# Kernel optimization log

Hardware: AMD Instinct MI355X
Metric: run time of the kernel (lower is better)

Reference implementation:

```python
import jax, jax.numpy as jnp
import numpy as np

TAU_PLUS = 0.02
TAU_MINUS = 0.02
TAU_X = 0.101
A_TRIPLET = 0.0065
HOMEOSTATIC_RATE = 0.1
DT = 0.001
SPIKE_P = 0.05  # spike probability used to binarize inputs


def setup_inputs() -> dict:
    key = jax.random.key(0)
    k1, k2, k3 = jax.random.split(key, 3)
    B, P, Q, T = 16, 2048, 2048, 256
    pre_spikes = (jax.random.uniform(k1, (B, P, T)) < SPIKE_P).astype(jnp.float32)
    post_spikes = (jax.random.uniform(k2, (B, Q, T)) < SPIKE_P).astype(jnp.float32)
    weights = jax.random.normal(k3, (P, Q), dtype=jnp.float32) * 0.1
    meta_A_plus = jnp.float32(0.01)
    meta_A_minus = jnp.float32(0.012)
    return {"pre_spikes": pre_spikes, "post_spikes": post_spikes,
            "weights": weights, "meta_A_plus": meta_A_plus,
            "meta_A_minus": meta_A_minus}


def _traces(spikes_tbn, decay):
    """Trace value used at step t: x_t = decay * (x_{t-1} + s_{t-1}), x_0 = 0."""
    def step(carry, s):
        x = decay * carry          # decayed trace, used for this step's update
        return x + s, x            # spike added AFTER the update, per original
    init = jnp.zeros(spikes_tbn.shape[1:], spikes_tbn.dtype)
    _, xs = jax.lax.scan(step, init, spikes_tbn)
    return xs  # [T, B, N]


def reference(pre_spikes, post_spikes, weights, meta_A_plus, meta_A_minus):
    B, P, T = pre_spikes.shape
    exp_plus = jnp.exp(jnp.float32(-DT / TAU_PLUS))
    exp_minus = jnp.exp(jnp.float32(-DT / TAU_MINUS))
    exp_x = jnp.exp(jnp.float32(-DT / TAU_X))

    pre_t = jnp.transpose(pre_spikes, (2, 0, 1))    # [T, B, P]
    post_t = jnp.transpose(post_spikes, (2, 0, 1))  # [T, B, Q]

    x_pre = _traces(pre_t, exp_plus)     # [T, B, P]
    x_post = _traces(post_t, exp_minus)  # [T, B, Q]
    x_trip = _traces(post_t, exp_x)      # [T, B, Q]

    # Per-step outer products summed over time == one big contraction over (t, b).
    ltp = jnp.einsum('tbp,tbq->pq', x_pre, post_t) * meta_A_plus
    triplet = jnp.einsum('tbp,tbq->pq', x_pre, post_t * x_trip) * A_TRIPLET
    ltd = jnp.einsum('tbp,tbq->pq', pre_t, x_post) * meta_A_minus
    weight_updates = ltp + triplet - ltd

    # Homeostatic scaling (fresh module: activity history holds only this sample)
    current_activity = (pre_spikes.sum() + post_spikes.sum()) / (B * T)
    scaling_factor = jnp.sqrt(HOMEOSTATIC_RATE / (current_activity + 1e-6))

    updated_weights = weights + weight_updates * scaling_factor
    return jnp.clip(updated_weights, -2.0, 2.0)
```

## Files before the change

### kernel.cpp

```cpp
#include <hip/hip_runtime.h>

constexpr int TB = 16;
constexpr int NP = 2048;
constexpr int NQ = 2048;
constexpr int TT = 256;
constexpr int KH = TB * TT;
constexpr int KT = 2 * KH;

typedef unsigned short ushort_t;
typedef __attribute__((ext_vector_type(8))) __bf16 bf16x8;
typedef __attribute__((ext_vector_type(4))) float f32x4;

__device__ __forceinline__ unsigned bf1(float f) {
    unsigned u = __builtin_bit_cast(unsigned, f);
    return (u + 0x7FFFu + ((u >> 16) & 1u)) >> 16;
}
__device__ __forceinline__ unsigned pack2(float lo, float hi) {
    return bf1(lo) | (bf1(hi) << 16);
}
__device__ __forceinline__ unsigned spk2(float a, float b) {
    return ((a != 0.f) ? 0x3F80u : 0u) | ((b != 0.f) ? 0x3F800000u : 0u);
}

constexpr float DF1 = 0.95122942450071400910f;
constexpr float DF2 = DF1 * DF1;
constexpr float DF4 = DF2 * DF2;
constexpr float DF8 = DF4 * DF4;
constexpr float DF16 = DF8 * DF8;
constexpr float DF32 = DF16 * DF16;
constexpr float DF64 = DF32 * DF32;
constexpr float DF128 = DF64 * DF64;

constexpr float DX1 = 0.99014786386058731819f;
constexpr float DX2 = DX1 * DX1;
constexpr float DX4 = DX2 * DX2;
constexpr float DX8 = DX4 * DX4;
constexpr float DX16 = DX8 * DX8;
constexpr float DX32 = DX16 * DX16;
constexpr float DX64 = DX32 * DX32;
constexpr float DX128 = DX64 * DX64;

template <int K>
__device__ __forceinline__ float seg_step(float b, float pw, int sl) {
    float t = __shfl_up(b, K, 64);
    return (sl >= K) ? fmaf(pw, t, b) : b;
}

__device__ __forceinline__ float fold4(float C, float4 u, float d) {
    C = d * (C + u.x); C = d * (C + u.y); C = d * (C + u.z); C = d * (C + u.w);
    return C;
}
__device__ __forceinline__ float4 expand4(float& x, float4 u, float d) {
    float4 t;
    t.x = x; x = d * (x + u.x);
    t.y = x; x = d * (x + u.y);
    t.z = x; x = d * (x + u.z);
    t.w = x; x = d * (x + u.w);
    return t;
}

__global__ __launch_bounds__(256) void stage_traces(
    const float* __restrict__ pre, const float* __restrict__ post,
    const float* __restrict__ mApP, const float* __restrict__ mAmP,
    ushort_t* __restrict__ Ab, ushort_t* __restrict__ Bb,
    float* __restrict__ partials)
{
    const int tid  = threadIdx.x;
    const int lane = tid & 63;
    const int wv   = tid >> 6;
    const int sl   = lane & 15;
    const int seg  = lane >> 4;
    const int rowg = blockIdx.x * 16 + wv * 4 + seg;
    const bool isPre = rowg < TB * NP;
    const int m = isPre ? rowg : rowg - TB * NP;
    const int b = m >> 11;
    const int r = m & 2047;

    const float4* src =
        (const float4*)((isPre ? pre : post) + (size_t)m * TT) + sl * 4;
    const float4 u0 = src[0], u1 = src[1], u2 = src[2], u3 = src[3];

    float cnt = ((u0.x + u0.y) + (u0.z + u0.w)) + ((u1.x + u1.y) + (u1.z + u1.w))
              + ((u2.x + u2.y) + (u2.z + u2.w)) + ((u3.x + u3.y) + (u3.z + u3.w));

    float Cf = fold4(fold4(fold4(fold4(0.f, u0, DF1), u1, DF1), u2, DF1), u3, DF1);
    float bs = Cf;
    bs = seg_step<1>(bs, DF16, sl);
    bs = seg_step<2>(bs, DF32, sl);
    bs = seg_step<4>(bs, DF64, sl);
    bs = seg_step<8>(bs, DF128, sl);
    float xinf = __shfl_up(bs, 1, 64);
    if (sl == 0) xinf = 0.f;

    float xm = xinf;
    const float4 t0 = expand4(xm, u0, DF1);
    const float4 t1 = expand4(xm, u1, DF1);
    const float4 t2 = expand4(xm, u2, DF1);
    const float4 t3 = expand4(xm, u3, DF1);

    uint4 va, va2, vb, vb2;
    if (isPre) {
        va  = uint4{pack2(t0.x, t0.y), pack2(t0.z, t0.w),
                    pack2(t1.x, t1.y), pack2(t1.z, t1.w)};
        va2 = uint4{pack2(t2.x, t2.y), pack2(t2.z, t2.w),
                    pack2(t3.x, t3.y), pack2(t3.z, t3.w)};
        vb  = uint4{spk2(u0.x, u0.y), spk2(u0.z, u0.w),
                    spk2(u1.x, u1.y), spk2(u1.z, u1.w)};
        vb2 = uint4{spk2(u2.x, u2.y), spk2(u2.z, u2.w),
                    spk2(u3.x, u3.y), spk2(u3.z, u3.w)};
    } else {
        float Cx = fold4(fold4(fold4(fold4(0.f, u0, DX1), u1, DX1), u2, DX1), u3, DX1);
        float bx = Cx;
        bx = seg_step<1>(bx, DX16, sl);
        bx = seg_step<2>(bx, DX32, sl);
        bx = seg_step<4>(bx, DX64, sl);
        bx = seg_step<8>(bx, DX128, sl);
        float xint = __shfl_up(bx, 1, 64);
        if (sl == 0) xint = 0.f;

        float xt = xint;
        const float4 w0 = expand4(xt, u0, DX1);
        const float4 w1 = expand4(xt, u1, DX1);
        const float4 w2 = expand4(xt, u2, DX1);
        const float4 w3 = expand4(xt, u3, DX1);

        const float Ap = *mApP;
        const float Am = *mAmP;
        auto av2 = [&](float sa, float ta, float sb, float tb) -> unsigned {
            unsigned lo = (sa != 0.f) ? bf1(fmaf(0.0065f, ta, Ap)) : 0u;
            unsigned hi = (sb != 0.f) ? bf1(fmaf(0.0065f, tb, Ap)) : 0u;
            return lo | (hi << 16);
        };
        va  = uint4{av2(u0.x, w0.x, u0.y, w0.y), av2(u0.z, w0.z, u0.w, w0.w),
                    av2(u1.x, w1.x, u1.y, w1.y), av2(u1.z, w1.z, u1.w, w1.w)};
        va2 = uint4{av2(u2.x, w2.x, u2.y, w2.y), av2(u2.z, w2.z, u2.w, w2.w),
                    av2(u3.x, w3.x, u3.y, w3.y), av2(u3.z, w3.z, u3.w, w3.w)};
        vb  = uint4{pack2(-Am * t0.x, -Am * t0.y), pack2(-Am * t0.z, -Am * t0.w),
                    pack2(-Am * t1.x, -Am * t1.y), pack2(-Am * t1.z, -Am * t1.w)};
        vb2 = uint4{pack2(-Am * t2.x, -Am * t2.y), pack2(-Am * t2.z, -Am * t2.w),
                    pack2(-Am * t3.x, -Am * t3.y), pack2(-Am * t3.z, -Am * t3.w)};
    }

    ushort_t* o0 = (isPre ? Ab : Bb) + (size_t)r * KT + b * TT + sl * 16;
    ((uint4*)o0)[0] = va;
    ((uint4*)o0)[1] = va2;
    ((uint4*)(o0 + KH))[0] = vb;
    ((uint4*)(o0 + KH))[1] = vb2;

    #pragma unroll
    for (int off = 32; off > 0; off >>= 1)
        cnt += __shfl_down(cnt, off, 64);
    __shared__ float wsum[4];
    if (lane == 0) wsum[wv] = cnt;
    __syncthreads();
    if (tid == 0) {
        float s = (wsum[0] + wsum[1]) + (wsum[2] + wsum[3]);
        atomicAdd(&partials[(blockIdx.x & 63) * 16], s);
    }
}

__device__ __forceinline__ void async16(const ushort_t* g, ushort_t* l) {
    __builtin_amdgcn_global_load_lds(
        (const __attribute__((address_space(1))) unsigned int*)g,
        (__attribute__((address_space(3))) unsigned int*)l,
        16, 0, 0);
}

__global__ __launch_bounds__(256, 2) void gemm_split(
    const ushort_t* __restrict__ Ab, const ushort_t* __restrict__ Bb,
    float* __restrict__ P0, float* __restrict__ P1)
{
    __shared__ ushort_t As[2][128 * 64];
    __shared__ ushort_t Bs[2][128 * 64];

    const int tid  = threadIdx.x;
    const int lane = tid & 63;
    const int wv   = tid >> 6;
    const int wr   = wv >> 1;
    const int wc   = wv & 1;
    const int quad = lane >> 4;
    const int m16  = lane & 15;

    const int id  = blockIdx.x;
    const int xcd = id & 7;
    const int j5  = id >> 3;
    const int z   = j5 & 1;
    const int t   = j5 >> 1;
    const int pt  = ((xcd >> 1) << 2) + (t >> 3);
    const int qt  = ((xcd & 1) << 3) + (t & 7);

    const int p0 = pt * 128;
    const int q0 = qt * 128;
    const int kbase = z * (KT / 2);
    const int ldsbase = wv * 512;

    const ushort_t* gaP[4];
    const ushort_t* gbP[4];
    #pragma unroll
    for (int rr = 0; rr < 4; ++rr) {
        const int c   = rr * 256 + tid;
        const int row = c >> 3;
        const int kk8 = (c & 7) ^ (row & 7);
        gaP[rr] = Ab + (size_t)(p0 + row) * KT + kbase + kk8 * 8;
        gbP[rr] = Bb + (size_t)(q0 + row) * KT + kbase + kk8 * 8;
    }

    f32x4 acc[4][4] = {};

    auto stageF = [&](int buf) {
        #pragma unroll
        for (int rr = 0; rr < 4; ++rr) {
            async16(gaP[rr], &As[buf][rr * 2048 + ldsbase]);
            async16(gbP[rr], &Bs[buf][rr * 2048 + ldsbase]);
            gaP[rr] += 64;
            gbP[rr] += 64;
        }
    };
    auto computeF = [&](int buf) {
        #pragma unroll
        for (int ks = 0; ks < 2; ++ks) {
            bf16x8 af[4], bf[4];
            #pragma unroll
            for (int i = 0; i < 4; ++i) {
                const int row  = wr * 64 + i * 16 + m16;
                const int slot = (ks * 4 + quad) ^ (row & 7);
                af[i] = *(const bf16x8*)&As[buf][row * 64 + slot * 8];
            }
            #pragma unroll
            for (int jj = 0; jj < 4; ++jj) {
                const int row  = wc * 64 + jj * 16 + m16;
                const int slot = (ks * 4 + quad) ^ (row & 7);
                bf[jj] = *(const bf16x8*)&Bs[buf][row * 64 + slot * 8];
            }
            #pragma unroll
            for (int i = 0; i < 4; ++i)
                #pragma unroll
                for (int jj = 0; jj < 4; ++jj)
                    acc[i][jj] = __builtin_amdgcn_mfma_f32_16x16x32_bf16(
                        af[i], bf[jj], acc[i][jj], 0, 0, 0);
        }
    };

    constexpr int NIT = (KT / 2) / 64;
    stageF(0);
    for (int kt2 = 0; kt2 < NIT / 2; ++kt2) {
        __syncthreads();
        stageF(1);
        computeF(0);
        __syncthreads();
        if (kt2 + 1 < NIT / 2)
            stageF(0);
        computeF(1);
    }

    float* P = z ? P1 : P0;
    #pragma unroll
    for (int i = 0; i < 4; ++i) {
        const int prow = p0 + wr * 64 + i * 16 + quad * 4;
        #pragma unroll
        for (int jj = 0; jj < 4; ++jj) {
            const int qcol = q0 + wc * 64 + jj * 16 + m16;
            #pragma unroll
            for (int r2 = 0; r2 < 4; ++r2)
                P[(size_t)(prow + r2) * NQ + qcol] = acc[i][jj][r2];
        }
    }
}

__global__ __launch_bounds__(256) void merge_out(
    const float* __restrict__ W, const float* __restrict__ P1,
    const float* __restrict__ partials, float* __restrict__ Out)
{
    __shared__ float s_scale;
    const int tid = threadIdx.x;
    if (tid < 64) {
        float v = partials[tid * 16];
        #pragma unroll
        for (int off = 32; off > 0; off >>= 1)
            v += __shfl_down(v, off, 64);
        if (tid == 0)
            s_scale = sqrtf(0.1f / (v * (1.0f / 4096.0f) + 1e-6f));
    }
    __syncthreads();
    const float scale = s_scale;

    const size_t i4 = (size_t)blockIdx.x * 256 + tid;
    float4 w = ((const float4*)W)[i4];
    float4 a = ((const float4*)Out)[i4];
    float4 c = ((const float4*)P1)[i4];
    float4 o;
    o.x = fminf(fmaxf(fmaf(scale, a.x + c.x, w.x), -2.f), 2.f);
    o.y = fminf(fmaxf(fmaf(scale, a.y + c.y, w.y), -2.f), 2.f);
    o.z = fminf(fmaxf(fmaf(scale, a.z + c.z, w.z), -2.f), 2.f);
    o.w = fminf(fmaxf(fmaf(scale, a.w + c.w, w.w), -2.f), 2.f);
    ((float4*)Out)[i4] = o;
}

extern "C" void kernel_launch(void* const* d_in, const int* in_sizes, int n_in,
                              void* d_out, int out_size, void* d_ws, size_t ws_size,
                              hipStream_t stream) {
    const float* pre  = (const float*)d_in[0];
    const float* post = (const float*)d_in[1];
    const float* W    = (const float*)d_in[2];
    const float* mAp  = (const float*)d_in[3];
    const float* mAm  = (const float*)d_in[4];
    float* out = (float*)d_out;

    char* ws = (char*)d_ws;
    float* partials = (float*)ws;
    ushort_t* Ab = (ushort_t*)(ws + 16384);
    ushort_t* Bb = (ushort_t*)(ws + 16384 + (size_t)NP * KT * 2);
    float* P1    = (float*)(ws + 16384 + 2 * (size_t)NP * KT * 2);

    hipMemsetAsync(partials, 0, 64 * 16 * sizeof(float), stream);

    stage_traces<<<dim3((TB * NP + TB * NQ) / 16), dim3(256), 0, stream>>>(
        pre, post, mAp, mAm, Ab, Bb, partials);

    gemm_split<<<dim3(512), dim3(256), 0, stream>>>(Ab, Bb, out, P1);

    merge_out<<<dim3(NP * NQ / 1024), dim3(256), 0, stream>>>(
        W, P1, partials, out);
}
```

Measured before the change: 205.9 us.

## Split GEMM K four ways with smaller K tiles and move scale reduction into GEMM

The GEMM now splits the K dimension into four partial sums instead of two and launches 1024 blocks. It uses 32-wide K tiles, which halves LDS per block and raises the launch bound to allow more blocks per CU. The activity sum now goes into per-block partials with no atomics or memset, and block 0 of the GEMM reduces them into a scale value. The aim is better occupancy and latency hiding, at the cost of two more 16 MB fp32 partial buffers written and re-read in the merge, plus more synchronisation per unit of K work.

```diff
diff --git a/kernel.cpp b/kernel.cpp
--- a/kernel.cpp
+++ b/kernel.cpp
@@ -153,10 +153,8 @@
     __shared__ float wsum[4];
     if (lane == 0) wsum[wv] = cnt;
     __syncthreads();
-    if (tid == 0) {
-        float s = (wsum[0] + wsum[1]) + (wsum[2] + wsum[3]);
-        atomicAdd(&partials[(blockIdx.x & 63) * 16], s);
-    }
+    if (tid == 0)
+        partials[blockIdx.x] = (wsum[0] + wsum[1]) + (wsum[2] + wsum[3]);
 }
 
 __device__ __forceinline__ void async16(const ushort_t* g, ushort_t* l) {
@@ -166,12 +164,15 @@
         16, 0, 0);
 }
 
-__global__ __launch_bounds__(256, 2) void gemm_split(
+__global__ __launch_bounds__(256, 5) void gemm_split(
     const ushort_t* __restrict__ Ab, const ushort_t* __restrict__ Bb,
-    float* __restrict__ P0, float* __restrict__ P1)
+    const float* __restrict__ sp, float* __restrict__ scaleBuf,
+    float* __restrict__ P0, float* __restrict__ P1,
+    float* __restrict__ P2, float* __restrict__ P3)
 {
-    __shared__ ushort_t As[2][128 * 64];
-    __shared__ ushort_t Bs[2][128 * 64];
+    __shared__ ushort_t As[2][128 * 32];
+    __shared__ ushort_t Bs[2][128 * 32];
+    __shared__ float red[4];
 
     const int tid  = threadIdx.x;
     const int lane = tid & 63;
@@ -181,67 +182,79 @@
     const int quad = lane >> 4;
     const int m16  = lane & 15;
 
+    if (blockIdx.x == 0) {
+        float v = 0.f;
+        #pragma unroll
+        for (int i = 0; i < 16; ++i) v += sp[tid + i * 256];
+        #pragma unroll
+        for (int off = 32; off > 0; off >>= 1)
+            v += __shfl_down(v, off, 64);
+        if (lane == 0) red[wv] = v;
+        __syncthreads();
+        if (tid == 0) {
+            float s = (red[0] + red[1]) + (red[2] + red[3]);
+            scaleBuf[0] = sqrtf(0.1f / (s * (1.0f / 4096.0f) + 1e-6f));
+        }
+    }
+
     const int id  = blockIdx.x;
     const int xcd = id & 7;
-    const int j5  = id >> 3;
-    const int z   = j5 & 1;
-    const int t   = j5 >> 1;
+    const int rest = id >> 3;
+    const int z   = rest & 3;
+    const int t   = rest >> 2;
     const int pt  = ((xcd >> 1) << 2) + (t >> 3);
     const int qt  = ((xcd & 1) << 3) + (t & 7);
 
     const int p0 = pt * 128;
     const int q0 = qt * 128;
-    const int kbase = z * (KT / 2);
+    const int kbase = z * (KT / 4);
     const int ldsbase = wv * 512;
 
-    const ushort_t* gaP[4];
-    const ushort_t* gbP[4];
+    const ushort_t* gaP[2];
+    const ushort_t* gbP[2];
     #pragma unroll
-    for (int rr = 0; rr < 4; ++rr) {
+    for (int rr = 0; rr < 2; ++rr) {
         const int c   = rr * 256 + tid;
-        const int row = c >> 3;
-        const int kk8 = (c & 7) ^ (row & 7);
-        gaP[rr] = Ab + (size_t)(p0 + row) * KT + kbase + kk8 * 8;
-        gbP[rr] = Bb + (size_t)(q0 + row) * KT + kbase + kk8 * 8;
+        const int row = c >> 2;
+        const int kk4 = (c & 3) ^ (row & 3);
+        gaP[rr] = Ab + (size_t)(p0 + row) * KT + kbase + kk4 * 8;
+        gbP[rr] = Bb + (size_t)(q0 + row) * KT + kbase + kk4 * 8;
     }
 
     f32x4 acc[4][4] = {};
 
     auto stageF = [&](int buf) {
         #pragma unroll
-        for (int rr = 0; rr < 4; ++rr) {
+        for (int rr = 0; rr < 2; ++rr) {
             async16(gaP[rr], &As[buf][rr * 2048 + ldsbase]);
             async16(gbP[rr], &Bs[buf][rr * 2048 + ldsbase]);
-            gaP[rr] += 64;
-            gbP[rr] += 64;
+            gaP[rr] += 32;
+            gbP[rr] += 32;
         }
     };
     auto computeF = [&](int buf) {
-        #pragma unroll
-        for (int ks = 0; ks < 2; ++ks) {
-            bf16x8 af[4], bf[4];
+        bf16x8 af[4], bf[4];
+        #pragma unroll
+        for (int i = 0; i < 4; ++i) {
+            const int row  = wr * 64 + i * 16 + m16;
+            const int slot = quad ^ (row & 3);
+            af[i] = *(const bf16x8*)&As[buf][row * 32 + slot * 8];
+        }
+        #pragma unroll
+        for (int jj = 0; jj < 4; ++jj) {
+            const int row  = wc * 64 + jj * 16 + m16;
+            const int slot = quad ^ (row & 3);
+            bf[jj] = *(const bf16x8*)&Bs[buf][row * 32 + slot * 8];
+        }
+        #pragma unroll
+        for (int i = 0; i < 4; ++i)
             #pragma unroll
-            for (int i = 0; i < 4; ++i) {
-                const int row  = wr * 64 + i * 16 + m16;
-                const int slot = (ks * 4 + quad) ^ (row & 7);
-                af[i] = *(const bf16x8*)&As[buf][row * 64 + slot * 8];
-            }
-            #pragma unroll
-            for (int jj = 0; jj < 4; ++jj) {
-                const int row  = wc * 64 + jj * 16 + m16;
-                const int slot = (ks * 4 + quad) ^ (row & 7);
-                bf[jj] = *(const bf16x8*)&Bs[buf][row * 64 + slot * 8];
-            }
-            #pragma unroll
-            for (int i = 0; i < 4; ++i)
-                #pragma unroll
-                for (int jj = 0; jj < 4; ++jj)
-                    acc[i][jj] = __builtin_amdgcn_mfma_f32_16x16x32_bf16(
-                        af[i], bf[jj], acc[i][jj], 0, 0, 0);
-        }
+            for (int jj = 0; jj < 4; ++jj)
+                acc[i][jj] = __builtin_amdgcn_mfma_f32_16x16x32_bf16(
+                    af[i], bf[jj], acc[i][jj], 0, 0, 0);
     };
 
-    constexpr int NIT = (KT / 2) / 64;
+    constexpr int NIT = (KT / 4) / 32;
     stageF(0);
     for (int kt2 = 0; kt2 < NIT / 2; ++kt2) {
         __syncthreads();
@@ -253,7 +266,7 @@
         computeF(1);
     }
 
-    float* P = z ? P1 : P0;
+    float* P = (z == 0) ? P0 : (z == 1) ? P1 : (z == 2) ? P2 : P3;
     #pragma unroll
     for (int i = 0; i < 4; ++i) {
         const int prow = p0 + wr * 64 + i * 16 + quad * 4;
@@ -268,31 +281,23 @@
 }
 
 __global__ __launch_bounds__(256) void merge_out(
-    const float* __restrict__ W, const float* __restrict__ P1,
-    const float* __restrict__ partials, float* __restrict__ Out)
+    const float* __restrict__ W,
+    const float* __restrict__ P1, const float* __restrict__ P2,
+    const float* __restrict__ P3, const float* __restrict__ scaleBuf,
+    float* __restrict__ Out)
 {
-    __shared__ float s_scale;
-    const int tid = threadIdx.x;
-    if (tid < 64) {
-        float v = partials[tid * 16];
-        #pragma unroll
-        for (int off = 32; off > 0; off >>= 1)
-            v += __shfl_down(v, off, 64);
-        if (tid == 0)
-            s_scale = sqrtf(0.1f / (v * (1.0f / 4096.0f) + 1e-6f));
-    }
-    __syncthreads();
-    const float scale = s_scale;
-
-    const size_t i4 = (size_t)blockIdx.x * 256 + tid;
+    const float scale = scaleBuf[0];
+    const size_t i4 = (size_t)blockIdx.x * 256 + threadIdx.x;
     float4 w = ((const float4*)W)[i4];
     float4 a = ((const float4*)Out)[i4];
-    float4 c = ((const float4*)P1)[i4];
+    float4 b = ((const float4*)P1)[i4];
+    float4 c = ((const float4*)P2)[i4];
+    float4 d = ((const float4*)P3)[i4];
     float4 o;
-    o.x = fminf(fmaxf(fmaf(scale, a.x + c.x, w.x), -2.f), 2.f);
-    o.y = fminf(fmaxf(fmaf(scale, a.y + c.y, w.y), -2.f), 2.f);
-    o.z = fminf(fmaxf(fmaf(scale, a.z + c.z, w.z), -2.f), 2.f);
-    o.w = fminf(fmaxf(fmaf(scale, a.w + c.w, w.w), -2.f), 2.f);
+    o.x = fminf(fmaxf(fmaf(scale, (a.x + b.x) + (c.x + d.x), w.x), -2.f), 2.f);
+    o.y = fminf(fmaxf(fmaf(scale, (a.y + b.y) + (c.y + d.y), w.y), -2.f), 2.f);
+    o.z = fminf(fmaxf(fmaf(scale, (a.z + b.z) + (c.z + d.z), w.z), -2.f), 2.f);
+    o.w = fminf(fmaxf(fmaf(scale, (a.w + b.w) + (c.w + d.w), w.w), -2.f), 2.f);
     ((float4*)Out)[i4] = o;
 }
 
@@ -308,17 +313,20 @@
 
     char* ws = (char*)d_ws;
     float* partials = (float*)ws;
-    ushort_t* Ab = (ushort_t*)(ws + 16384);
-    ushort_t* Bb = (ushort_t*)(ws + 16384 + (size_t)NP * KT * 2);
-    float* P1    = (float*)(ws + 16384 + 2 * (size_t)NP * KT * 2);
-
-    hipMemsetAsync(partials, 0, 64 * 16 * sizeof(float), stream);
+    float* scaleBuf = (float*)(ws + 16384);
+    ushort_t* Ab = (ushort_t*)(ws + 32768);
+    ushort_t* Bb = (ushort_t*)(ws + 32768 + (size_t)NP * KT * 2);
+    char* pbase  = ws + 32768 + 2 * (size_t)NP * KT * 2;
+    float* P1 = (float*)pbase;
+    float* P2 = (float*)(pbase + (size_t)NP * NQ * 4);
+    float* P3 = (float*)(pbase + 2 * (size_t)NP * NQ * 4);
 
     stage_traces<<<dim3((TB * NP + TB * NQ) / 16), dim3(256), 0, stream>>>(
         pre, post, mAp, mAm, Ab, Bb, partials);
 
-    gemm_split<<<dim3(512), dim3(256), 0, stream>>>(Ab, Bb, out, P1);
+    gemm_split<<<dim3(1024), dim3(256), 0, stream>>>(
+        Ab, Bb, partials, scaleBuf, out, P1, P2, P3);
 
     merge_out<<<dim3(NP * NQ / 1024), dim3(256), 0, stream>>>(
-        W, P1, partials, out);
-}
+        W, P1, P2, P3, scaleBuf, out);
+}
```

Measured after the change: 249.0 us. +20.9%, slower.

## Coalesce trace-stage loads and stores, drop memset and atomics for homeostatic sum

Applied to the files above, without the earlier changes.

The trace kernel now has each of the 16 lanes per row load interleaved float4 chunks, so a warp touches contiguous memory. It computes four independent 64-step segment scans and stitches them together with shuffles and decay powers. The activity count goes to a per-block partials array with a plain store instead of an atomicAdd. That removes the memset launch, and block 0 of the GEMM reduces the partials into a scale value that merge_out reads directly. The cost is more shuffles and a serial reduction on one GEMM block, plus 8-byte stores in place of 16-byte ones.

```diff
diff --git a/kernel.cpp b/kernel.cpp
--- a/kernel.cpp
+++ b/kernel.cpp
@@ -29,7 +29,6 @@
 constexpr float DF16 = DF8 * DF8;
 constexpr float DF32 = DF16 * DF16;
 constexpr float DF64 = DF32 * DF32;
-constexpr float DF128 = DF64 * DF64;
 
 constexpr float DX1 = 0.99014786386058731819f;
 constexpr float DX2 = DX1 * DX1;
@@ -38,24 +37,32 @@
 constexpr float DX16 = DX8 * DX8;
 constexpr float DX32 = DX16 * DX16;
 constexpr float DX64 = DX32 * DX32;
-constexpr float DX128 = DX64 * DX64;
 
 template <int K>
 __device__ __forceinline__ float seg_step(float b, float pw, int sl) {
     float t = __shfl_up(b, K, 64);
     return (sl >= K) ? fmaf(pw, t, b) : b;
 }
-
-__device__ __forceinline__ float fold4(float C, float4 u, float d) {
-    C = d * (C + u.x); C = d * (C + u.y); C = d * (C + u.z); C = d * (C + u.w);
+__device__ __forceinline__ float scan16(float c, float p1, float p2, float p4,
+                                        float p8, int sl) {
+    c = seg_step<1>(c, p1, sl);
+    c = seg_step<2>(c, p2, sl);
+    c = seg_step<4>(c, p4, sl);
+    c = seg_step<8>(c, p8, sl);
+    return c;
+}
+
+__device__ __forceinline__ float fold4(float4 u, float d) {
+    float C = d * u.x;
+    C = d * (C + u.y); C = d * (C + u.z); C = d * (C + u.w);
     return C;
 }
-__device__ __forceinline__ float4 expand4(float& x, float4 u, float d) {
+__device__ __forceinline__ float4 expand4(float x, float4 u, float d) {
     float4 t;
     t.x = x; x = d * (x + u.x);
     t.y = x; x = d * (x + u.y);
     t.z = x; x = d * (x + u.z);
-    t.w = x; x = d * (x + u.w);
+    t.w = x;
     return t;
 }
 
@@ -69,83 +76,101 @@
     const int lane = tid & 63;
     const int wv   = tid >> 6;
     const int sl   = lane & 15;
-    const int seg  = lane >> 4;
-    const int rowg = blockIdx.x * 16 + wv * 4 + seg;
+    const int rowg = blockIdx.x * 16 + wv * 4 + (lane >> 4);
     const bool isPre = rowg < TB * NP;
     const int m = isPre ? rowg : rowg - TB * NP;
     const int b = m >> 11;
     const int r = m & 2047;
 
-    const float4* src =
-        (const float4*)((isPre ? pre : post) + (size_t)m * TT) + sl * 4;
-    const float4 u0 = src[0], u1 = src[1], u2 = src[2], u3 = src[3];
+    const float4* srcRow = (const float4*)((isPre ? pre : post) + (size_t)m * TT);
+    const float4 u0 = srcRow[sl];
+    const float4 u1 = srcRow[16 + sl];
+    const float4 u2 = srcRow[32 + sl];
+    const float4 u3 = srcRow[48 + sl];
 
     float cnt = ((u0.x + u0.y) + (u0.z + u0.w)) + ((u1.x + u1.y) + (u1.z + u1.w))
               + ((u2.x + u2.y) + (u2.z + u2.w)) + ((u3.x + u3.y) + (u3.z + u3.w));
 
-    float Cf = fold4(fold4(fold4(fold4(0.f, u0, DF1), u1, DF1), u2, DF1), u3, DF1);
-    float bs = Cf;
-    bs = seg_step<1>(bs, DF16, sl);
-    bs = seg_step<2>(bs, DF32, sl);
-    bs = seg_step<4>(bs, DF64, sl);
-    bs = seg_step<8>(bs, DF128, sl);
-    float xinf = __shfl_up(bs, 1, 64);
-    if (sl == 0) xinf = 0.f;
-
-    float xm = xinf;
-    const float4 t0 = expand4(xm, u0, DF1);
-    const float4 t1 = expand4(xm, u1, DF1);
-    const float4 t2 = expand4(xm, u2, DF1);
-    const float4 t3 = expand4(xm, u3, DF1);
-
-    uint4 va, va2, vb, vb2;
+    const int hi = lane | 15;
+
+    float bf0 = scan16(fold4(u0, DF1), DF4, DF8, DF16, DF32, sl);
+    float bf1_ = scan16(fold4(u1, DF1), DF4, DF8, DF16, DF32, sl);
+    float bf2 = scan16(fold4(u2, DF1), DF4, DF8, DF16, DF32, sl);
+    float bf3 = scan16(fold4(u3, DF1), DF4, DF8, DF16, DF32, sl);
+    const float Tf0 = __shfl(bf0, hi, 64);
+    const float Tf1 = __shfl(bf1_, hi, 64);
+    const float Tf2 = __shfl(bf2, hi, 64);
+    const float Xf1 = Tf0;
+    const float Xf2 = fmaf(DF64, Xf1, Tf1);
+    const float Xf3 = fmaf(DF64, Xf2, Tf2);
+    float ef0 = __shfl_up(bf0, 1, 64);
+    float ef1 = __shfl_up(bf1_, 1, 64);
+    float ef2 = __shfl_up(bf2, 1, 64);
+    float ef3 = __shfl_up(bf3, 1, 64);
+    if (sl == 0) { ef0 = 0.f; ef1 = 0.f; ef2 = 0.f; ef3 = 0.f; }
+    float pf = 1.f;
+    if (sl & 1) pf *= DF4;
+    if (sl & 2) pf *= DF8;
+    if (sl & 4) pf *= DF16;
+    if (sl & 8) pf *= DF32;
+    const float4 t0 = expand4(ef0,                 u0, DF1);
+    const float4 t1 = expand4(fmaf(pf, Xf1, ef1),  u1, DF1);
+    const float4 t2 = expand4(fmaf(pf, Xf2, ef2),  u2, DF1);
+    const float4 t3 = expand4(fmaf(pf, Xf3, ef3),  u3, DF1);
+
+    ushort_t* oA = (isPre ? Ab : Bb) + (size_t)r * KT + b * TT + 4 * sl;
+
     if (isPre) {
-        va  = uint4{pack2(t0.x, t0.y), pack2(t0.z, t0.w),
-                    pack2(t1.x, t1.y), pack2(t1.z, t1.w)};
-        va2 = uint4{pack2(t2.x, t2.y), pack2(t2.z, t2.w),
-                    pack2(t3.x, t3.y), pack2(t3.z, t3.w)};
-        vb  = uint4{spk2(u0.x, u0.y), spk2(u0.z, u0.w),
-                    spk2(u1.x, u1.y), spk2(u1.z, u1.w)};
-        vb2 = uint4{spk2(u2.x, u2.y), spk2(u2.z, u2.w),
-                    spk2(u3.x, u3.y), spk2(u3.z, u3.w)};
+        *(uint2*)(oA)            = uint2{pack2(t0.x, t0.y), pack2(t0.z, t0.w)};
+        *(uint2*)(oA + 64)       = uint2{pack2(t1.x, t1.y), pack2(t1.z, t1.w)};
+        *(uint2*)(oA + 128)      = uint2{pack2(t2.x, t2.y), pack2(t2.z, t2.w)};
+        *(uint2*)(oA + 192)      = uint2{pack2(t3.x, t3.y), pack2(t3.z, t3.w)};
+        *(uint2*)(oA + KH)       = uint2{spk2(u0.x, u0.y), spk2(u0.z, u0.w)};
+        *(uint2*)(oA + KH + 64)  = uint2{spk2(u1.x, u1.y), spk2(u1.z, u1.w)};
+        *(uint2*)(oA + KH + 128) = uint2{spk2(u2.x, u2.y), spk2(u2.z, u2.w)};
+        *(uint2*)(oA + KH + 192) = uint2{spk2(u3.x, u3.y), spk2(u3.z, u3.w)};
     } else {
-        float Cx = fold4(fold4(fold4(fold4(0.f, u0, DX1), u1, DX1), u2, DX1), u3, DX1);
-        float bx = Cx;
-        bx = seg_step<1>(bx, DX16, sl);
-        bx = seg_step<2>(bx, DX32, sl);
-        bx = seg_step<4>(bx, DX64, sl);
-        bx = seg_step<8>(bx, DX128, sl);
-        float xint = __shfl_up(bx, 1, 64);
-        if (sl == 0) xint = 0.f;
-
-        float xt = xint;
-        const float4 w0 = expand4(xt, u0, DX1);
-        const float4 w1 = expand4(xt, u1, DX1);
-        const float4 w2 = expand4(xt, u2, DX1);
-        const float4 w3 = expand4(xt, u3, DX1);
+        float bx0 = scan16(fold4(u0, DX1), DX4, DX8, DX16, DX32, sl);
+        float bx1 = scan16(fold4(u1, DX1), DX4, DX8, DX16, DX32, sl);
+        float bx2 = scan16(fold4(u2, DX1), DX4, DX8, DX16, DX32, sl);
+        float bx3 = scan16(fold4(u3, DX1), DX4, DX8, DX16, DX32, sl);
+        const float Tx0 = __shfl(bx0, hi, 64);
+        const float Tx1 = __shfl(bx1, hi, 64);
+        const float Tx2 = __shfl(bx2, hi, 64);
+        const float Xx1 = Tx0;
+        const float Xx2 = fmaf(DX64, Xx1, Tx1);
+        const float Xx3 = fmaf(DX64, Xx2, Tx2);
+        float ex0 = __shfl_up(bx0, 1, 64);
+        float ex1 = __shfl_up(bx1, 1, 64);
+        float ex2 = __shfl_up(bx2, 1, 64);
+        float ex3 = __shfl_up(bx3, 1, 64);
+        if (sl == 0) { ex0 = 0.f; ex1 = 0.f; ex2 = 0.f; ex3 = 0.f; }
+        float px = 1.f;
+        if (sl & 1) px *= DX4;
+        if (sl & 2) px *= DX8;
+        if (sl & 4) px *= DX16;
+        if (sl & 8) px *= DX32;
+        const float4 w0 = expand4(ex0,                u0, DX1);
+        const float4 w1 = expand4(fmaf(px, Xx1, ex1), u1, DX1);
+        const float4 w2 = expand4(fmaf(px, Xx2, ex2), u2, DX1);
+        const float4 w3 = expand4(fmaf(px, Xx3, ex3), u3, DX1);
 
         const float Ap = *mApP;
         const float Am = *mAmP;
         auto av2 = [&](float sa, float ta, float sb, float tb) -> unsigned {
             unsigned lo = (sa != 0.f) ? bf1(fmaf(0.0065f, ta, Ap)) : 0u;
-            unsigned hi = (sb != 0.f) ? bf1(fmaf(0.0065f, tb, Ap)) : 0u;
-            return lo | (hi << 16);
+            unsigned hi2 = (sb != 0.f) ? bf1(fmaf(0.0065f, tb, Ap)) : 0u;
+            return lo | (hi2 << 16);
         };
-        va  = uint4{av2(u0.x, w0.x, u0.y, w0.y), av2(u0.z, w0.z, u0.w, w0.w),
-                    av2(u1.x, w1.x, u1.y, w1.y), av2(u1.z, w1.z, u1.w, w1.w)};
-        va2 = uint4{av2(u2.x, w2.x, u2.y, w2.y), av2(u2.z, w2.z, u2.w, w2.w),
-                    av2(u3.x, w3.x, u3.y, w3.y), av2(u3.z, w3.z, u3.w, w3.w)};
-        vb  = uint4{pack2(-Am * t0.x, -Am * t0.y), pack2(-Am * t0.z, -Am * t0.w),
-                    pack2(-Am * t1.x, -Am * t1.y), pack2(-Am * t1.z, -Am * t1.w)};
-        vb2 = uint4{pack2(-Am * t2.x, -Am * t2.y), pack2(-Am * t2.z, -Am * t2.w),
-                    pack2(-Am * t3.x, -Am * t3.y), pack2(-Am * t3.z, -Am * t3.w)};
-    }
-
-    ushort_t* o0 = (isPre ? Ab : Bb) + (size_t)r * KT + b * TT + sl * 16;
-    ((uint4*)o0)[0] = va;
-    ((uint4*)o0)[1] = va2;
-    ((uint4*)(o0 + KH))[0] = vb;
-    ((uint4*)(o0 + KH))[1] = vb2;
+        *(uint2*)(oA)       = uint2{av2(u0.x, w0.x, u0.y, w0.y), av2(u0.z, w0.z, u0.w, w0.w)};
+        *(uint2*)(oA + 64)  = uint2{av2(u1.x, w1.x, u1.y, w1.y), av2(u1.z, w1.z, u1.w, w1.w)};
+        *(uint2*)(oA + 128) = uint2{av2(u2.x, w2.x, u2.y, w2.y), av2(u2.z, w2.z, u2.w, w2.w)};
+        *(uint2*)(oA + 192) = uint2{av2(u3.x, w3.x, u3.y, w3.y), av2(u3.z, w3.z, u3.w, w3.w)};
+        *(uint2*)(oA + KH)       = uint2{pack2(-Am * t0.x, -Am * t0.y), pack2(-Am * t0.z, -Am * t0.w)};
+        *(uint2*)(oA + KH + 64)  = uint2{pack2(-Am * t1.x, -Am * t1.y), pack2(-Am * t1.z, -Am * t1.w)};
+        *(uint2*)(oA + KH + 128) = uint2{pack2(-Am * t2.x, -Am * t2.y), pack2(-Am * t2.z, -Am * t2.w)};
+        *(uint2*)(oA + KH + 192) = uint2{pack2(-Am * t3.x, -Am * t3.y), pack2(-Am * t3.z, -Am * t3.w)};
+    }
 
     #pragma unroll
     for (int off = 32; off > 0; off >>= 1)
@@ -153,10 +178,8 @@
     __shared__ float wsum[4];
     if (lane == 0) wsum[wv] = cnt;
     __syncthreads();
-    if (tid == 0) {
-        float s = (wsum[0] + wsum[1]) + (wsum[2] + wsum[3]);
-        atomicAdd(&partials[(blockIdx.x & 63) * 16], s);
-    }
+    if (tid == 0)
+        partials[blockIdx.x] = (wsum[0] + wsum[1]) + (wsum[2] + wsum[3]);
 }
 
 __device__ __forceinline__ void async16(const ushort_t* g, ushort_t* l) {
@@ -168,10 +191,12 @@
 
 __global__ __launch_bounds__(256, 2) void gemm_split(
     const ushort_t* __restrict__ Ab, const ushort_t* __restrict__ Bb,
+    const float* __restrict__ sp, float* __restrict__ scaleBuf,
     float* __restrict__ P0, float* __restrict__ P1)
 {
     __shared__ ushort_t As[2][128 * 64];
     __shared__ ushort_t Bs[2][128 * 64];
+    __shared__ float red[4];
 
     const int tid  = threadIdx.x;
     const int lane = tid & 63;
@@ -180,6 +205,21 @@
     const int wc   = wv & 1;
     const int quad = lane >> 4;
     const int m16  = lane & 15;
+
+    if (blockIdx.x == 0) {
+        float v = 0.f;
+        #pragma unroll
+        for (int i = 0; i < 16; ++i) v += sp[tid + i * 256];
+        #pragma unroll
+        for (int off = 32; off > 0; off >>= 1)
+            v += __shfl_down(v, off, 64);
+        if (lane == 0) red[wv] = v;
+        __syncthreads();
+        if (tid == 0) {
+            float s = (red[0] + red[1]) + (red[2] + red[3]);
+            scaleBuf[0] = sqrtf(0.1f / (s * (1.0f / 4096.0f) + 1e-6f));
+        }
+    }
 
     const int id  = blockIdx.x;
     const int xcd = id & 7;
@@ -269,22 +309,10 @@
 
 __global__ __launch_bounds__(256) void merge_out(
     const float* __restrict__ W, const float* __restrict__ P1,
-    const float* __restrict__ partials, float* __restrict__ Out)
+    const float* __restrict__ scaleBuf, float* __restrict__ Out)
 {
-    __shared__ float s_scale;
-    const int tid = threadIdx.x;
-    if (tid < 64) {
-        float v = partials[tid * 16];
-        #pragma unroll
-        for (int off = 32; off > 0; off >>= 1)
-            v += __shfl_down(v, off, 64);
-        if (tid == 0)
-            s_scale = sqrtf(0.1f / (v * (1.0f / 4096.0f) + 1e-6f));
-    }
-    __syncthreads();
-    const float scale = s_scale;
-
-    const size_t i4 = (size_t)blockIdx.x * 256 + tid;
+    const float scale = scaleBuf[0];
+    const size_t i4 = (size_t)blockIdx.x * 256 + threadIdx.x;
     float4 w = ((const float4*)W)[i4];
     float4 a = ((const float4*)Out)[i4];
     float4 c = ((const float4*)P1)[i4];
@@ -308,17 +336,17 @@
 
     char* ws = (char*)d_ws;
     float* partials = (float*)ws;
-    ushort_t* Ab = (ushort_t*)(ws + 16384);
-    ushort_t* Bb = (ushort_t*)(ws + 16384 + (size_t)NP * KT * 2);
-    float* P1    = (float*)(ws + 16384 + 2 * (size_t)NP * KT * 2);
-
-    hipMemsetAsync(partials, 0, 64 * 16 * sizeof(float), stream);
+    float* scaleBuf = (float*)(ws + 16384);
+    ushort_t* Ab = (ushort_t*)(ws + 32768);
+    ushort_t* Bb = (ushort_t*)(ws + 32768 + (size_t)NP * KT * 2);
+    float* P1    = (float*)(ws + 32768 + 2 * (size_t)NP * KT * 2);
 
     stage_traces<<<dim3((TB * NP + TB * NQ) / 16), dim3(256), 0, stream>>>(
         pre, post, mAp, mAm, Ab, Bb, partials);
 
-    gemm_split<<<dim3(512), dim3(256), 0, stream>>>(Ab, Bb, out, P1);
+    gemm_split<<<dim3(512), dim3(256), 0, stream>>>(
+        Ab, Bb, partials, scaleBuf, out, P1);
 
     merge_out<<<dim3(NP * NQ / 1024), dim3(256), 0, stream>>>(
-        W, P1, partials, out);
-}
+        W, P1, scaleBuf, out);
+}
```

Measured after the change: 199.6 us. 1.03x faster.
